# Kernel tuning notes

Hardware: AMD Instinct MI355X
Metric: run time of the kernel (lower is better)

## Reference

```python
import jax, jax.numpy as jnp
import numpy as np

LN_EPS = 1e-5

def _proj(x, w, b):
    # 1x1 conv: x [B,C,H,W], w [O,C], b [O]
    return jnp.einsum('bchw,oc->bohw', x, w) + b[None, :, None, None]

def _layernorm(x, w, b):
    # normalize over last dim
    mu = jnp.mean(x, axis=-1, keepdims=True)
    var = jnp.mean(jnp.square(x - mu), axis=-1, keepdims=True)
    return (x - mu) * jax.lax.rsqrt(var + LN_EPS) * w + b

def setup_inputs() -> dict:
    key = jax.random.key(0)
    ks = jax.random.split(key, 12)
    C = 256
    d = {
        's3': jax.random.normal(ks[0], (2, C, 64, 64), jnp.float32),
        's4': jax.random.normal(ks[1], (2, C, 32, 64), jnp.float32),
        's5': jax.random.normal(ks[2], (2, C, 16, 64), jnp.float32),
        'qw': jax.random.normal(ks[3], (C, C), jnp.float32) * 0.02,
        'qb': jax.random.normal(ks[4], (C,), jnp.float32) * 0.02,
        'kw': jax.random.normal(ks[5], (C, C), jnp.float32) * 0.02,
        'kb': jax.random.normal(ks[6], (C,), jnp.float32) * 0.02,
        'vw': jax.random.normal(ks[7], (C, C), jnp.float32) * 0.02,
        'vb': jax.random.normal(ks[8], (C,), jnp.float32) * 0.02,
        'ow': jax.random.normal(ks[9], (C, C), jnp.float32) * 0.02,
        'ob': jax.random.normal(ks[10], (C,), jnp.float32) * 0.02,
        'ln_w': jnp.ones((C,), jnp.float32),
        'ln_b': jnp.zeros((C,), jnp.float32),
    }
    return d

def reference(s3, s4, s5, qw, qb, kw, kb, vw, vb, ow, ob, ln_w, ln_b):
    B, C, H, W = s3.shape
    num_heads = 8
    head_dim = C // num_heads
    scale = head_dim ** -0.5

    q = _proj(s3, qw, qb).reshape(B, C, H * W)            # [B,C,Nq]
    k4 = _proj(s4, kw, kb).reshape(B, C, -1)
    k5 = _proj(s5, kw, kb).reshape(B, C, -1)
    v4 = _proj(s4, vw, vb).reshape(B, C, -1)
    v5 = _proj(s5, vw, vb).reshape(B, C, -1)
    k = jnp.concatenate([k4, k5], axis=-1)                # [B,C,Nk]
    v = jnp.concatenate([v4, v5], axis=-1)

    # [B,C,N] -> [B,h,N,d]
    def split_heads(t):
        Bn, Cn, N = t.shape
        return t.transpose(0, 2, 1).reshape(Bn, N, num_heads, head_dim).transpose(0, 2, 1, 3)

    qh, kh, vh = split_heads(q), split_heads(k), split_heads(v)
    attn = jnp.einsum('bhqd,bhkd->bhqk', qh, kh) * scale
    attn = jax.nn.softmax(attn, axis=-1)
    out = jnp.einsum('bhqk,bhkd->bhqd', attn, vh)         # [B,h,Nq,d]
    out = out.transpose(0, 2, 1, 3).reshape(B, H * W, C)  # [B,Nq,C]
    out = out.transpose(0, 2, 1).reshape(B, C, H, W)
    out = _proj(out, ow, ob)
    out = s3 + out
    out_flat = out.reshape(B, C, H * W).transpose(0, 2, 1)  # [B,N,C]
    out_flat = _layernorm(out_flat, ln_w, ln_b)
    return out_flat.transpose(0, 2, 1).reshape(B, C, H, W)
```

## Files before the change

kernel.cpp:

```cpp
#include <hip/hip_runtime.h>

typedef __bf16 bf16;
typedef __bf16 bf16x4 __attribute__((ext_vector_type(4)));
typedef __bf16 bf16x8 __attribute__((ext_vector_type(8)));
typedef _Float16 f16;
typedef _Float16 f16x2 __attribute__((ext_vector_type(2)));
typedef _Float16 f16x4 __attribute__((ext_vector_type(4)));
typedef _Float16 f16x8 __attribute__((ext_vector_type(8)));
typedef float f32x4 __attribute__((ext_vector_type(4)));
typedef unsigned int u32x4 __attribute__((ext_vector_type(4)));

#define MFMA16 __builtin_amdgcn_mfma_f32_16x16x32_bf16
#define MFMA16H __builtin_amdgcn_mfma_f32_16x16x32_f16

__device__ __forceinline__ void async16(void* lds, const void* g) {
    __builtin_amdgcn_global_load_lds((const __attribute__((address_space(1))) unsigned int*)g,
                                     (__attribute__((address_space(3))) unsigned int*)lds, 16, 0, 0);
}

__device__ __forceinline__ f16x2 pkrtz(float a, float b) {
    return __builtin_bit_cast(f16x2, __builtin_amdgcn_cvt_pkrtz(a, b));
}

__device__ __forceinline__ float fdot2h(f16x2 a, f16x2 b, float c) {
#if __has_builtin(__builtin_amdgcn_fdot2)
    return __builtin_amdgcn_fdot2(a, b, c, false);
#else
    return c + (float)a[0] * (float)b[0] + (float)a[1] * (float)b[1];
#endif
}

__global__ __launch_bounds__(256) void k_prep(const float* __restrict__ qw, const float* __restrict__ kw,
                                              const float* __restrict__ vw, const float* __restrict__ ow,
                                              bf16* __restrict__ Wb,
                                              const float* __restrict__ s3, const float* __restrict__ s4,
                                              const float* __restrict__ s5,
                                              bf16* __restrict__ s3t, bf16* __restrict__ s45t) {
    __shared__ float T[64][65];
    int bx = blockIdx.x, t = threadIdx.x;
    if (bx < 256) {
        int tt = bx * 256 + t;
        const float* srcs[4] = {qw, kw, vw, ow};
        int which = tt >> 14;
        int idx = (tt & 16383) * 4;
        f32x4 v = *(const f32x4*)(srcs[which] + idx);
        bf16x4 o;
        o[0] = (bf16)v[0]; o[1] = (bf16)v[1]; o[2] = (bf16)v[2]; o[3] = (bf16)v[3];
        *(bf16x4*)(Wb + (size_t)which * 65536 + idx) = o;
        return;
    }
    const float* src; bf16* dst; int N, dstRows, rowOff, x, y, z;
    if (bx < 768)       { int i = bx - 256;  src = s3; dst = s3t;  N = 4096; dstRows = 4096; rowOff = 0;    x = i & 63; y = (i >> 6) & 3; z = i >> 8; }
    else if (bx < 1024) { int i = bx - 768;  src = s4; dst = s45t; N = 2048; dstRows = 3072; rowOff = 0;    x = i & 31; y = (i >> 5) & 3; z = i >> 7; }
    else                { int i = bx - 1024; src = s5; dst = s45t; N = 1024; dstRows = 3072; rowOff = 2048; x = i & 15; y = (i >> 4) & 3; z = i >> 6; }
    int c0 = y * 64, n0 = x * 64, b = z;
    const float* s = src + ((size_t)b * 256 + c0) * N + n0;
#pragma unroll
    for (int i = 0; i < 4; i++) {
        int flat = i * 256 + t;
        int row = flat >> 4;
        int col = (flat & 15) * 4;
        f32x4 v = *(const f32x4*)(s + (size_t)row * N + col);
        T[row][col + 0] = v[0]; T[row][col + 1] = v[1];
        T[row][col + 2] = v[2]; T[row][col + 3] = v[3];
    }
    __syncthreads();
#pragma unroll
    for (int i = 0; i < 4; i++) {
        int flat = i * 256 + t;
        int nrow = flat >> 4;
        int c4 = (flat & 15) * 4;
        bf16x4 o;
        o[0] = (bf16)T[c4 + 0][nrow]; o[1] = (bf16)T[c4 + 1][nrow];
        o[2] = (bf16)T[c4 + 2][nrow]; o[3] = (bf16)T[c4 + 3][nrow];
        *(bf16x4*)(dst + ((size_t)(b * dstRows + rowOff + n0 + nrow)) * 256 + c0 + c4) = o;
    }
}

__global__ __launch_bounds__(256) void k_qkv(const bf16* __restrict__ Wb,
                                             const bf16* __restrict__ s3t, const bf16* __restrict__ s45t,
                                             const float* __restrict__ qb, const float* __restrict__ kb,
                                             const float* __restrict__ vb,
                                             bf16* __restrict__ Qb, bf16* __restrict__ Kb,
                                             f16* __restrict__ Vtb, float qscale) {
    int i = blockIdx.x;
    int mode, n0, m0, b, Nrows;
    const bf16 *A, *Bt; const float* bias; float oscale = 1.0f;
    if (i < 512) {
        mode = 0; A = Wb; Bt = s3t; bias = qb; Nrows = 4096; oscale = qscale;
        n0 = (i & 63) * 64; m0 = ((i >> 6) & 3) * 64; b = i >> 8;
    } else if (i < 896) {
        unsigned j = i - 512;
        mode = 1; A = Wb + 65536; Bt = s45t; bias = kb; Nrows = 3072;
        n0 = (j % 48u) * 64; unsigned rr = j / 48u; m0 = (rr & 3) * 64; b = rr >> 2;
    } else {
        unsigned j = i - 896;
        mode = 2; A = Wb + 131072; Bt = s45t; bias = vb; Nrows = 3072;
        n0 = (j % 48u) * 64; unsigned rr = j / 48u; m0 = (rr & 3) * 64; b = rr >> 2;
    }
    __shared__ __align__(16) bf16 As[2][64 * 32];
    __shared__ __align__(16) bf16 Bs[2][64 * 32];
    int t = threadIdx.x;
    int w = t >> 6, lane = t & 63;
    int lrow = lane & 15, lk = lane >> 4;
    f32x4 acc[4] = {};
    const bf16* Ag = A + (size_t)(m0 + w * 16 + (lane >> 2)) * 256 + (lane & 3) * 8;
    const bf16* Bg = Bt + ((size_t)b * Nrows + n0 + w * 16 + (lane >> 2)) * 256 + (lane & 3) * 8;
    async16(&As[0][w * 512], Ag);
    async16(&Bs[0][w * 512], Bg);
    __syncthreads();
    for (int s8 = 0; s8 < 8; ++s8) {
        int buf = s8 & 1;
        if (s8 < 7) {
            async16(&As[buf ^ 1][w * 512], Ag + (s8 + 1) * 32);
            async16(&Bs[buf ^ 1][w * 512], Bg + (s8 + 1) * 32);
        }
        bf16x8 af = *(const bf16x8*)(&As[buf][(w * 16 + lrow) * 32 + lk * 8]);
#pragma unroll
        for (int ct = 0; ct < 4; ct++) {
            bf16x8 bfr = *(const bf16x8*)(&Bs[buf][(ct * 16 + lrow) * 32 + lk * 8]);
            acc[ct] = MFMA16(af, bfr, acc[ct], 0, 0, 0);
        }
        __syncthreads();
    }
    int o0 = m0 + w * 16 + lk * 4;
    f32x4 b4 = *(const f32x4*)(bias + o0);
    int head = o0 >> 5;
#pragma unroll
    for (int ct = 0; ct < 4; ct++) {
        int n = n0 + ct * 16 + lrow;
        if (mode == 0) {
            int dd = o0 & 31;
            bf16x4 pv;
#pragma unroll
            for (int j = 0; j < 4; j++) pv[j] = (bf16)((acc[ct][j] + b4[j]) * oscale);
            *(bf16x4*)(Qb + ((size_t)(b * 8 + head) * 4096 + n) * 32 + dd) = pv;
        } else if (mode == 1) {
            int dd = o0 & 31;
            int u = n & 31;
            int np = (n & ~31) | (((u >> 2) & 1) << 4) | ((u >> 3) << 2) | (u & 3);
            bf16x4 pv;
#pragma unroll
            for (int j = 0; j < 4; j++) pv[j] = (bf16)(acc[ct][j] + b4[j]);
            *(bf16x4*)(Kb + ((size_t)(b * 8 + head) * 3072 + np) * 32 + dd) = pv;
        } else {
            int g = (n & 63) >> 3;
#pragma unroll
            for (int j = 0; j < 4; j++) {
                int dd = (o0 & 31) + j;
                int col = (n & ~63) + ((g ^ (dd & 7)) << 3) + (n & 7);
                Vtb[((size_t)(b * 8 + head) * 32 + dd) * 3072 + col] = (f16)(acc[ct][j] + b4[j]);
            }
        }
    }
}

__global__ __launch_bounds__(256, 4) void k_attn(const bf16* __restrict__ Q, const bf16* __restrict__ K,
                                                 const f16* __restrict__ Vt,
                                                 f16* __restrict__ Opart, float* __restrict__ Lsum) {
    int id = blockIdx.x;
    int bh = id & 15;
    int sp = (id >> 4) & 1;
    int q0 = (id >> 5) * 128;
    int kn0 = sp * 1536;
    int t = threadIdx.x, w = t >> 6, lane = t & 63;
    int lrow = lane & 15, lk = lane >> 4;
    __shared__ __align__(16) char smem[32768];
    bf16* Ks = (bf16*)smem;
    f16* Vs = (f16*)(smem + 16384);
    f16* Tq = (f16*)smem;
    const bf16* kbase = K + (size_t)bh * 3072 * 32;
    const f16* vbase = Vt + (size_t)bh * 32 * 3072;
    const bf16* kg = kbase + (size_t)(kn0 + w * 16 + (lane >> 2)) * 32 + (lane & 3) * 8;
    const f16* vg = vbase + (size_t)(w * 8 + (lane >> 3)) * 3072 + kn0 + (lane & 7) * 8;
    bf16x8 aq[2];
#pragma unroll
    for (int qg = 0; qg < 2; ++qg)
        aq[qg] = *(const bf16x8*)(Q + ((size_t)bh * 4096 + q0 + w * 32 + qg * 16 + lrow) * 32 + lk * 8);
    f32x4 accO[2][2] = {};
    float lsum[2] = {0.f, 0.f};
    f32x4 zero = {};
    f16x2 one2; one2[0] = (f16)1.f; one2[1] = (f16)1.f;
    int vkey = lrow & 7;
    async16(Ks + w * 512, kg);
    async16(Ks + 2048 + w * 512, kg + 64 * 32);
    async16(Vs + w * 512, vg);
    async16(Vs + 2048 + w * 512, vg + 64);
    __syncthreads();
    for (int c = 0; c < 12; ++c) {
        int buf = c & 1;
        if (c < 11) {
            const bf16* kn_ = kg + (size_t)(c + 1) * 128 * 32;
            const f16* vn_ = vg + (c + 1) * 128;
            async16(Ks + (buf ^ 1) * 4096 + w * 512, kn_);
            async16(Ks + (buf ^ 1) * 4096 + 2048 + w * 512, kn_ + 64 * 32);
            async16(Vs + (buf ^ 1) * 4096 + w * 512, vn_);
            async16(Vs + (buf ^ 1) * 4096 + 2048 + w * 512, vn_ + 64);
        }
        const bf16* ksb = Ks + buf * 4096;
        const f16* vsb0 = Vs + buf * 4096;
#pragma unroll
        for (int p = 0; p < 4; ++p) {
            f32x4 s[2][2];
#pragma unroll
            for (int t2 = 0; t2 < 2; ++t2) {
                bf16x8 kf = *(const bf16x8*)(ksb + (p * 32 + t2 * 16 + lrow) * 32 + lk * 8);
#pragma unroll
                for (int qg = 0; qg < 2; ++qg) s[t2][qg] = MFMA16(kf, aq[qg], zero, 0, 0, 0);
            }
            const f16* vsb = vsb0 + (p >> 1) * 2048;
            int gran = (((p & 1) << 2) | lk) ^ vkey;
            f16x8 vf0 = *(const f16x8*)(vsb + lrow * 64 + (gran << 3));
            f16x8 vf1 = *(const f16x8*)(vsb + (16 + lrow) * 64 + (gran << 3));
#pragma unroll
            for (int qg = 0; qg < 2; ++qg) {
                f16x2 h0 = pkrtz(__builtin_amdgcn_exp2f(s[0][qg][0]), __builtin_amdgcn_exp2f(s[0][qg][1]));
                f16x2 h1 = pkrtz(__builtin_amdgcn_exp2f(s[0][qg][2]), __builtin_amdgcn_exp2f(s[0][qg][3]));
                f16x2 h2 = pkrtz(__builtin_amdgcn_exp2f(s[1][qg][0]), __builtin_amdgcn_exp2f(s[1][qg][1]));
                f16x2 h3 = pkrtz(__builtin_amdgcn_exp2f(s[1][qg][2]), __builtin_amdgcn_exp2f(s[1][qg][3]));
                f16x8 pk;
                pk[0] = h0[0]; pk[1] = h0[1]; pk[2] = h1[0]; pk[3] = h1[1];
                pk[4] = h2[0]; pk[5] = h2[1]; pk[6] = h3[0]; pk[7] = h3[1];
                lsum[qg] = fdot2h(h0, one2, lsum[qg]);
                lsum[qg] = fdot2h(h1, one2, lsum[qg]);
                lsum[qg] = fdot2h(h2, one2, lsum[qg]);
                lsum[qg] = fdot2h(h3, one2, lsum[qg]);
                accO[qg][0] = MFMA16H(vf0, pk, accO[qg][0], 0, 0, 0);
                accO[qg][1] = MFMA16H(vf1, pk, accO[qg][1], 0, 0, 0);
            }
        }
        __syncthreads();
    }
    int sb = sp * 16 + bh;
#pragma unroll
    for (int qg = 0; qg < 2; ++qg) {
        lsum[qg] += __shfl_xor(lsum[qg], 16, 64);
        lsum[qg] += __shfl_xor(lsum[qg], 32, 64);
    }
    if (lane < 16) {
#pragma unroll
        for (int qg = 0; qg < 2; ++qg)
            Lsum[(size_t)sb * 4096 + q0 + w * 32 + qg * 16 + lane] = lsum[qg];
    }
    f16* tw = Tq + w * 1088;
#pragma unroll
    for (int qg = 0; qg < 2; ++qg)
#pragma unroll
        for (int dh = 0; dh < 2; ++dh)
#pragma unroll
            for (int i = 0; i < 4; ++i)
                tw[(dh * 16 + lk * 4 + i) * 34 + qg * 16 + lrow] = (f16)accO[qg][dh][i];
    int q2 = (lane & 15) * 2, dgrp = (lane >> 4) * 8;
#pragma unroll
    for (int qq = 0; qq < 2; ++qq) {
        f16x8 ov;
#pragma unroll
        for (int dj = 0; dj < 8; ++dj) ov[dj] = tw[(dgrp + dj) * 34 + q2 + qq];
        *(f16x8*)(Opart + ((size_t)sb * 4096 + q0 + w * 32 + q2 + qq) * 32 + dgrp) = ov;
    }
}

__global__ __launch_bounds__(256) void k_oln(const bf16* __restrict__ A, const f16* __restrict__ Opart,
                                             const float* __restrict__ Ls, const float* __restrict__ bias,
                                             const bf16* __restrict__ s3t,
                                             const float* __restrict__ lnw, const float* __restrict__ lnb,
                                             float* __restrict__ out) {
    int i = blockIdx.x;
    int b = i >> 7, n0 = (i & 127) * 32;
    __shared__ __align__(16) char smem[34176];
    bf16* As = (bf16*)smem;
    bf16* Bs = (bf16*)(smem + 20480);
    float* T = (float*)smem;
    float* ps = (float*)(smem + 32896);
    float* pq = (float*)(smem + 33408);
    float* mu_s = (float*)(smem + 33920);
    float* rs_s = (float*)(smem + 34048);
    int t = threadIdx.x, w = t >> 6, lane = t & 63;
    int lrow = lane & 15, lk = lane >> 4;
    f32x4 acc[4][2] = {};
    int rB = t >> 3, cgB = (t & 7) * 4;
    int q = n0 + rB;
    const size_t SPS = (size_t)16 * 4096 * 32;
    for (int kc = 0; kc < 256; kc += 32) {
        int bh = b * 8 + (kc >> 5);
        const bf16* ar = A + (size_t)t * 256 + kc;
        u32x4 va0 = *(const u32x4*)(ar);
        u32x4 va1 = *(const u32x4*)(ar + 8);
        u32x4 va2 = *(const u32x4*)(ar + 16);
        u32x4 va3 = *(const u32x4*)(ar + 24);
        float l = Ls[(size_t)bh * 4096 + q] + Ls[(size_t)(16 + bh) * 4096 + q];
        float rl = 1.0f / l;
        const f16* obp = Opart + ((size_t)bh * 4096 + q) * 32 + cgB;
        f16x4 a0 = *(const f16x4*)(obp);
        f16x4 a1 = *(const f16x4*)(obp + SPS);
        bf16x4 bb;
#pragma unroll
        for (int j = 0; j < 4; ++j) bb[j] = (bf16)(((float)a0[j] + (float)a1[j]) * rl);
        *(u32x4*)(As + t * 40 + 0) = va0;
        *(u32x4*)(As + t * 40 + 8) = va1;
        *(u32x4*)(As + t * 40 + 16) = va2;
        *(u32x4*)(As + t * 40 + 24) = va3;
        *(bf16x4*)(Bs + rB * 40 + cgB) = bb;
        __syncthreads();
#pragma unroll
        for (int mt = 0; mt < 4; ++mt) {
            bf16x8 af = *(const bf16x8*)(As + (mt * 64 + w * 16 + lrow) * 40 + lk * 8);
#pragma unroll
            for (int ct = 0; ct < 2; ++ct) {
                bf16x8 bfr = *(const bf16x8*)(Bs + (ct * 16 + lrow) * 40 + lk * 8);
                acc[mt][ct] = MFMA16(af, bfr, acc[mt][ct], 0, 0, 0);
            }
        }
        __syncthreads();
    }
    float wsum[2] = {0.f, 0.f}, wsq[2] = {0.f, 0.f};
#pragma unroll
    for (int ct = 0; ct < 2; ++ct) {
        int n = ct * 16 + lrow;
#pragma unroll
        for (int mt = 0; mt < 4; ++mt) {
            int c0 = mt * 64 + w * 16 + lk * 4;
            f32x4 b4 = *(const f32x4*)(bias + c0);
            bf16x4 rv = *(const bf16x4*)(s3t + ((size_t)b * 4096 + n0 + n) * 256 + c0);
#pragma unroll
            for (int j = 0; j < 4; ++j) {
                float v = acc[mt][ct][j] + b4[j] + (float)rv[j];
                T[n * 257 + c0 + j] = v;
                wsum[ct] += v;
                wsq[ct] += v * v;
            }
        }
    }
#pragma unroll
    for (int ct = 0; ct < 2; ++ct) {
        wsum[ct] += __shfl_xor(wsum[ct], 16, 64);
        wsum[ct] += __shfl_xor(wsum[ct], 32, 64);
        wsq[ct] += __shfl_xor(wsq[ct], 16, 64);
        wsq[ct] += __shfl_xor(wsq[ct], 32, 64);
    }
    if (lk == 0) {
#pragma unroll
        for (int ct = 0; ct < 2; ++ct) {
            ps[w * 32 + ct * 16 + lrow] = wsum[ct];
            pq[w * 32 + ct * 16 + lrow] = wsq[ct];
        }
    }
    __syncthreads();
    if (t < 32) {
        float S = ps[t] + ps[32 + t] + ps[64 + t] + ps[96 + t];
        float Q2 = pq[t] + pq[32 + t] + pq[64 + t] + pq[96 + t];
        float m = S * (1.0f / 256.0f);
        mu_s[t] = m;
        rs_s[t] = rsqrtf(Q2 * (1.0f / 256.0f) - m * m + 1e-5f);
    }
    __syncthreads();
    int cb = t >> 3, n4 = (t & 7) * 4;
#pragma unroll
    for (int cc8 = 0; cc8 < 8; ++cc8) {
        int c = cb + cc8 * 32;
        float wv = lnw[c], bv = lnb[c];
        f32x4 o;
#pragma unroll
        for (int k2 = 0; k2 < 4; ++k2)
            o[k2] = (T[(n4 + k2) * 257 + c] - mu_s[n4 + k2]) * rs_s[n4 + k2] * wv + bv;
        *(f32x4*)(out + ((size_t)b * 256 + c) * 4096 + n0 + n4) = o;
    }
}

extern "C" void kernel_launch(void* const* d_in, const int* in_sizes, int n_in,
                              void* d_out, int out_size, void* d_ws, size_t ws_size,
                              hipStream_t stream) {
    const float* s3  = (const float*)d_in[0];
    const float* s4  = (const float*)d_in[1];
    const float* s5  = (const float*)d_in[2];
    const float* qw  = (const float*)d_in[3];
    const float* qb  = (const float*)d_in[4];
    const float* kw  = (const float*)d_in[5];
    const float* kb  = (const float*)d_in[6];
    const float* vw  = (const float*)d_in[7];
    const float* vb  = (const float*)d_in[8];
    const float* ow  = (const float*)d_in[9];
    const float* ob  = (const float*)d_in[10];
    const float* lnw = (const float*)d_in[11];
    const float* lnb = (const float*)d_in[12];
    float* out = (float*)d_out;
    char* ws = (char*)d_ws;

    bf16* Wb    = (bf16*)(ws);
    bf16* s3t   = (bf16*)(ws + (512ull << 10));
    bf16* s45t  = (bf16*)(ws + (4608ull << 10));
    bf16* Qb    = (bf16*)(ws + (7680ull << 10));
    bf16* Kb    = Qb + (2ull * 8 * 4096 * 32);
    f16*  Vtb   = (f16*)(Kb + (2ull * 8 * 3072 * 32));
    f16*  Opart = (f16*)(ws + (17920ull << 10));
    float* Lsum = (float*)(ws + (34304ull << 10));

    const float qscale = 0.17677669529663688f * 1.4426950408889634f;

    k_prep<<<1152, 256, 0, stream>>>(qw, kw, vw, ow, Wb, s3, s4, s5, s3t, s45t);
    k_qkv<<<1280, 256, 0, stream>>>(Wb, s3t, s45t, qb, kb, vb, Qb, Kb, Vtb, qscale);
    k_attn<<<1024, 256, 0, stream>>>(Qb, Kb, Vtb, Opart, Lsum);
    k_oln<<<256, 256, 0, stream>>>(Wb + 196608, Opart, Lsum, ob, s3t, lnw, lnb, out);
}
```

Before: 147.7 us.

## Deepen async LDS prefetch pipeline with explicit vmcnt waits in projection and attention

After: 149.6 us. No clear change (+1.3%).

```diff
diff --git a/kernel.cpp b/kernel.cpp
--- a/kernel.cpp
+++ b/kernel.cpp
@@ -108,20 +108,25 @@
     const bf16* Bg = Bt + ((size_t)b * Nrows + n0 + w * 16 + (lane >> 2)) * 256 + (lane & 3) * 8;
     async16(&As[0][w * 512], Ag);
     async16(&Bs[0][w * 512], Bg);
-    __syncthreads();
+    async16(&As[1][w * 512], Ag + 32);
+    async16(&Bs[1][w * 512], Bg + 32);
     for (int s8 = 0; s8 < 8; ++s8) {
         int buf = s8 & 1;
-        if (s8 < 7) {
-            async16(&As[buf ^ 1][w * 512], Ag + (s8 + 1) * 32);
-            async16(&Bs[buf ^ 1][w * 512], Bg + (s8 + 1) * 32);
-        }
+        if (s8 < 7) asm volatile("s_waitcnt vmcnt(2)" ::: "memory");
+        else        asm volatile("s_waitcnt vmcnt(0)" ::: "memory");
+        __builtin_amdgcn_s_barrier();
+        __builtin_amdgcn_sched_barrier(0);
         bf16x8 af = *(const bf16x8*)(&As[buf][(w * 16 + lrow) * 32 + lk * 8]);
 #pragma unroll
         for (int ct = 0; ct < 4; ct++) {
             bf16x8 bfr = *(const bf16x8*)(&Bs[buf][(ct * 16 + lrow) * 32 + lk * 8]);
             acc[ct] = MFMA16(af, bfr, acc[ct], 0, 0, 0);
         }
-        __syncthreads();
+        __builtin_amdgcn_s_barrier();
+        if (s8 < 6) {
+            async16(&As[buf][w * 512], Ag + (s8 + 2) * 32);
+            async16(&Bs[buf][w * 512], Bg + (s8 + 2) * 32);
+        }
     }
     int o0 = m0 + w * 16 + lk * 4;
     f32x4 b4 = *(const f32x4*)(bias + o0);
@@ -186,17 +191,20 @@
     async16(Ks + 2048 + w * 512, kg + 64 * 32);
     async16(Vs + w * 512, vg);
     async16(Vs + 2048 + w * 512, vg + 64);
-    __syncthreads();
+    {
+        const bf16* kn_ = kg + 128 * 32;
+        const f16* vn_ = vg + 128;
+        async16(Ks + 4096 + w * 512, kn_);
+        async16(Ks + 4096 + 2048 + w * 512, kn_ + 64 * 32);
+        async16(Vs + 4096 + w * 512, vn_);
+        async16(Vs + 4096 + 2048 + w * 512, vn_ + 64);
+    }
     for (int c = 0; c < 12; ++c) {
         int buf = c & 1;
-        if (c < 11) {
-            const bf16* kn_ = kg + (size_t)(c + 1) * 128 * 32;
-            const f16* vn_ = vg + (c + 1) * 128;
-            async16(Ks + (buf ^ 1) * 4096 + w * 512, kn_);
-            async16(Ks + (buf ^ 1) * 4096 + 2048 + w * 512, kn_ + 64 * 32);
-            async16(Vs + (buf ^ 1) * 4096 + w * 512, vn_);
-            async16(Vs + (buf ^ 1) * 4096 + 2048 + w * 512, vn_ + 64);
-        }
+        if (c < 11) asm volatile("s_waitcnt vmcnt(4)" ::: "memory");
+        else        asm volatile("s_waitcnt vmcnt(0)" ::: "memory");
+        __builtin_amdgcn_s_barrier();
+        __builtin_amdgcn_sched_barrier(0);
         const bf16* ksb = Ks + buf * 4096;
         const f16* vsb0 = Vs + buf * 4096;
 #pragma unroll
@@ -229,7 +237,15 @@
                 accO[qg][1] = MFMA16H(vf1, pk, accO[qg][1], 0, 0, 0);
             }
         }
-        __syncthreads();
+        __builtin_amdgcn_s_barrier();
+        if (c < 10) {
+            const bf16* kn_ = kg + (size_t)(c + 2) * 128 * 32;
+            const f16* vn_ = vg + (c + 2) * 128;
+            async16(Ks + buf * 4096 + w * 512, kn_);
+            async16(Ks + buf * 4096 + 2048 + w * 512, kn_ + 64 * 32);
+            async16(Vs + buf * 4096 + w * 512, vn_);
+            async16(Vs + buf * 4096 + 2048 + w * 512, vn_ + 64);
+        }
     }
     int sb = sp * 16 + bh;
 #pragma unroll
```
